# Performance work log

Hardware: AMD Instinct MI355X
Metric: run time of the kernel (lower is better)

Reference implementation:

```python
import jax, jax.numpy as jnp
import numpy as np

B, C_IN, C_OUT, H, W = 32, 64, 64, 128, 128
K, KH, KW = 4, 3, 3
HID = max(8, C_IN // 4)  # reduction=4 -> 16


def setup_inputs() -> dict:
    key = jax.random.key(0)
    ks = jax.random.split(key, 16)
    s = lambda k, shape, scale=0.1: jax.random.normal(k, shape, dtype=jnp.float32) * scale
    inp = {
        "x": jax.random.normal(ks[0], (B, C_IN, H, W), dtype=jnp.float32),
        "weight": s(ks[1], (K, C_OUT, C_IN, KH, KW)),  # static weight bank
        "bias": s(ks[2], (C_OUT,)),
        "mlp_w": s(ks[3], (HID, C_IN)),
        "mlp_b": s(ks[4], (HID,)),
        "wK": s(ks[5], (K, HID)),  "bK": s(ks[6], (K,)),
        "wO": s(ks[7], (C_OUT, HID)), "bO": s(ks[8], (C_OUT,)),
        "wI": s(ks[9], (C_IN, HID)),  "bI": s(ks[10], (C_IN,)),
        "wH": s(ks[11], (KH, HID)),   "bH": s(ks[12], (KH,)),
        "wW": s(ks[13], (KW, HID)),   "bW": s(ks[14], (KW,)),
    }
    return inp


def reference(x, weight, bias, mlp_w, mlp_b, wK, bK, wO, bO, wI, bI, wH, bH, wW, bW):
    # ---- attention branch: global avg pool -> MLP -> 5 heads ----
    g = jnp.mean(x, axis=(2, 3))                         # [B, C_in]
    h = jax.nn.relu(g @ mlp_w.T + mlp_b)                 # [B, HID]
    aK = jax.nn.softmax(h @ wK.T + bK, axis=1)           # [B, K]
    aO = jax.nn.sigmoid(h @ wO.T + bO)                   # [B, O]
    aI = jax.nn.sigmoid(h @ wI.T + bI)                   # [B, I]
    aH = jax.nn.sigmoid(h @ wH.T + bH)                   # [B, kh]
    aW = jax.nn.sigmoid(h @ wW.T + bW)                   # [B, kw]
    aH = aH / (jnp.sum(aH, axis=1, keepdims=True) + 1e-6)
    aW = aW / (jnp.sum(aW, axis=1, keepdims=True) + 1e-6)
    # fused 5-way outer product + reduction over K (same math as alpha einsum)
    w_dyn = jnp.einsum('bk,bo,bi,bh,bw,koihw->boihw', aK, aO, aI, aH, aW, weight)
    # ---- per-sample conv2d (groups=B trick expressed as vmap) ----
    def conv_one(xb, wb):
        return jax.lax.conv_general_dilated(
            xb[None], wb, window_strides=(1, 1), padding=((1, 1), (1, 1)),
            dimension_numbers=('NCHW', 'OIHW', 'NCHW'))[0]
    out = jax.vmap(conv_one)(x, w_dyn) + bias[None, :, None, None]
    return out
```

## Files before the change

### kernel.cpp

```cpp
#include <hip/hip_runtime.h>
#include <hip/hip_bf16.h>
#include <math.h>

#define BB 32
#define CI 64
#define CO 64
#define HH 128
#define WW 128
#define KK 4
#define HID 16

typedef __attribute__((ext_vector_type(8)))  __bf16 bf16x8;
typedef __attribute__((ext_vector_type(16))) float  floatx16;

__device__ __forceinline__ unsigned short f2bf(float f) {
    union { float f; unsigned int u; } a; a.f = f;
    unsigned int u = a.u;
    unsigned int r = (u + 0x7fffu + ((u >> 16) & 1u)) >> 16;
    return (unsigned short)r;
}

__global__ __launch_bounds__(256) void pool_kernel(const float* __restrict__ x,
                                                   float* __restrict__ g) {
    int bc = blockIdx.x;
    const float4* p = reinterpret_cast<const float4*>(x + (size_t)bc * (HH * WW));
    float s = 0.f;
    for (int i = threadIdx.x; i < (HH * WW) / 4; i += 256) {
        float4 v = p[i];
        s += v.x + v.y + v.z + v.w;
    }
    for (int off = 32; off > 0; off >>= 1) s += __shfl_down(s, off, 64);
    __shared__ float red[4];
    if ((threadIdx.x & 63) == 0) red[threadIdx.x >> 6] = s;
    __syncthreads();
    if (threadIdx.x == 0) {
        float tot = red[0] + red[1] + red[2] + red[3];
        g[bc] = tot * (1.0f / (HH * WW));
    }
}

__global__ __launch_bounds__(64) void attn_kernel(
    const float* __restrict__ g,
    const float* __restrict__ mlp_w, const float* __restrict__ mlp_b,
    const float* __restrict__ wK, const float* __restrict__ bK,
    const float* __restrict__ wO, const float* __restrict__ bO,
    const float* __restrict__ wI, const float* __restrict__ bI,
    const float* __restrict__ wH, const float* __restrict__ bH,
    const float* __restrict__ wW, const float* __restrict__ bW,
    float* __restrict__ aK, float* __restrict__ aO, float* __restrict__ aI,
    float* __restrict__ aH, float* __restrict__ aW) {
    int b = blockIdx.x;
    int t = threadIdx.x;
    __shared__ float sg[CI];
    __shared__ float sh[HID];
    __shared__ float sK[KK];
    __shared__ float sH[3];
    __shared__ float sW[3];

    sg[t] = g[b * CI + t];
    __syncthreads();

    if (t < HID) {
        float s = mlp_b[t];
        for (int c = 0; c < CI; c++) s = fmaf(mlp_w[t * CI + c], sg[c], s);
        sh[t] = fmaxf(s, 0.f);
    }
    __syncthreads();

    {
        float sO = bO[t], sI = bI[t];
        for (int j = 0; j < HID; j++) {
            float hv = sh[j];
            sO = fmaf(wO[t * HID + j], hv, sO);
            sI = fmaf(wI[t * HID + j], hv, sI);
        }
        aO[b * CO + t] = 1.f / (1.f + expf(-sO));
        aI[b * CI + t] = 1.f / (1.f + expf(-sI));
    }
    if (t < KK) {
        float s = bK[t];
        for (int j = 0; j < HID; j++) s = fmaf(wK[t * HID + j], sh[j], s);
        sK[t] = s;
    }
    if (t < 3) {
        float s = bH[t];
        for (int j = 0; j < HID; j++) s = fmaf(wH[t * HID + j], sh[j], s);
        sH[t] = 1.f / (1.f + expf(-s));
        float s2 = bW[t];
        for (int j = 0; j < HID; j++) s2 = fmaf(wW[t * HID + j], sh[j], s2);
        sW[t] = 1.f / (1.f + expf(-s2));
    }
    __syncthreads();

    if (t == 0) {
        float m = fmaxf(fmaxf(sK[0], sK[1]), fmaxf(sK[2], sK[3]));
        float e0 = expf(sK[0] - m), e1 = expf(sK[1] - m);
        float e2 = expf(sK[2] - m), e3 = expf(sK[3] - m);
        float s = e0 + e1 + e2 + e3;
        aK[b * KK + 0] = e0 / s;
        aK[b * KK + 1] = e1 / s;
        aK[b * KK + 2] = e2 / s;
        aK[b * KK + 3] = e3 / s;
        float hs = sH[0] + sH[1] + sH[2] + 1e-6f;
        float wsum = sW[0] + sW[1] + sW[2] + 1e-6f;
        for (int i = 0; i < 3; i++) {
            aH[b * 3 + i] = sH[i] / hs;
            aW[b * 3 + i] = sW[i] / wsum;
        }
    }
}

#define WD_TOT (BB * 9 * CO * CI)
__global__ __launch_bounds__(256) void wdyn_kernel(
    const float* __restrict__ weight,
    const float* __restrict__ aK, const float* __restrict__ aO,
    const float* __restrict__ aI, const float* __restrict__ aH,
    const float* __restrict__ aW, unsigned short* __restrict__ wdbf) {
    int idx = blockIdx.x * 256 + threadIdx.x;
    if (idx >= WD_TOT) return;
    int i   = idx & 63;
    int o   = (idx >> 6) & 63;
    int bt  = idx >> 12;
    int tap = bt % 9;
    int b   = bt / 9;

    int wbase = (o * CI + i) * 9 + tap;
    const float* ak = aK + b * KK;
    float s = 0.f;
#pragma unroll
    for (int k = 0; k < KK; k++) s = fmaf(ak[k], weight[k * (CO * CI * 9) + wbase], s);
    float v = s * aO[b * CO + o] * aI[b * CI + i] *
              aH[b * 3 + tap / 3] * aW[b * 3 + tap % 3];
    wdbf[idx] = f2bf(v);
}

#define ICCH 16
#define PADI 24
#define SX_ELE (6 * 130 * PADI)
#define SW_ELE (9 * 64 * PADI)

__global__ __launch_bounds__(512, 4) void conv_kernel(
    const float* __restrict__ x, const unsigned short* __restrict__ wdbf,
    const float* __restrict__ bias, float* __restrict__ out) {
    const int y0 = blockIdx.x * 4;
    const int b  = blockIdx.y;
    const int t  = threadIdx.x;
    const int lane = t & 63;
    const int w    = t >> 6;
    const int ry   = w >> 1;
    const int c0   = (w & 1) * 64;
    const int l31  = lane & 31;
    const int koct = lane >> 5;

    __shared__ __align__(16) unsigned short sx[SX_ELE];
    __shared__ __align__(16) unsigned short sw[SW_ELE];

    floatx16 acc[2][2];
#pragma unroll
    for (int i = 0; i < 2; i++)
#pragma unroll
        for (int j = 0; j < 2; j++)
#pragma unroll
            for (int q = 0; q < 16; q++) acc[i][j][q] = 0.f;

    const float* xb = x + (size_t)b * CI * HH * WW;
    const unsigned short* wdb = wdbf + (size_t)b * 9 * CO * CI;

    const int pA0 = (0 * 32 + l31) * PADI + koct * 8;
    const int pA1 = (1 * 32 + l31) * PADI + koct * 8;
    const int pB0 = (ry * 130 + c0 + 0  + l31) * PADI + koct * 8;
    const int pB1 = (ry * 130 + c0 + 32 + l31) * PADI + koct * 8;

    for (int chunk = 0; chunk < 4; chunk++) {
        const int ic0 = chunk * ICCH;
        __syncthreads();
        for (int idx = t; idx < 6 * 130 * 8; idx += 512) {
            int c  = idx % 130;
            int t2 = idx / 130;
            int r  = t2 % 6;
            int icp = t2 / 6;
            int gy = y0 - 1 + r;
            int gx = c - 1;
            float f0 = 0.f, f1 = 0.f;
            if ((unsigned)gy < (unsigned)HH && (unsigned)gx < (unsigned)WW) {
                const float* xp = xb + (size_t)(ic0 + icp * 2) * (HH * WW) + gy * WW + gx;
                f0 = xp[0];
                f1 = xp[HH * WW];
            }
            unsigned int pk = (unsigned int)f2bf(f0) | ((unsigned int)f2bf(f1) << 16);
            *reinterpret_cast<unsigned int*>(&sx[(r * 130 + c) * PADI + icp * 2]) = pk;
        }
        for (int idx = t; idx < 9 * 64 * 2; idx += 512) {
            int k8  = idx & 1;
            int oc  = (idx >> 1) & 63;
            int tap = idx >> 7;
            const uint4 v = *reinterpret_cast<const uint4*>(
                wdb + ((tap * 64 + oc) * 64 + ic0 + k8 * 8));
            *reinterpret_cast<uint4*>(&sw[(tap * 64 + oc) * PADI + k8 * 8]) = v;
        }
        __syncthreads();

#pragma unroll
        for (int kh = 0; kh < 3; kh++) {
#pragma unroll
            for (int kw = 0; kw < 3; kw++) {
                const int tap  = kh * 3 + kw;
                const int aoff = tap * (64 * PADI);
                const int boff = (kh * 130 + kw) * PADI;
                bf16x8 a0 = *reinterpret_cast<const bf16x8*>(&sw[pA0 + aoff]);
                bf16x8 a1 = *reinterpret_cast<const bf16x8*>(&sw[pA1 + aoff]);
                bf16x8 b0 = *reinterpret_cast<const bf16x8*>(&sx[pB0 + boff]);
                bf16x8 b1 = *reinterpret_cast<const bf16x8*>(&sx[pB1 + boff]);
                acc[0][0] = __builtin_amdgcn_mfma_f32_32x32x16_bf16(a0, b0, acc[0][0], 0, 0, 0);
                acc[0][1] = __builtin_amdgcn_mfma_f32_32x32x16_bf16(a0, b1, acc[0][1], 0, 0, 0);
                acc[1][0] = __builtin_amdgcn_mfma_f32_32x32x16_bf16(a1, b0, acc[1][0], 0, 0, 0);
                acc[1][1] = __builtin_amdgcn_mfma_f32_32x32x16_bf16(a1, b1, acc[1][1], 0, 0, 0);
            }
        }
    }

    const int y = y0 + ry;
    float* ob = out + (size_t)b * CO * HH * WW + (size_t)y * WW;
#pragma unroll
    for (int mt = 0; mt < 2; mt++) {
#pragma unroll
        for (int r = 0; r < 16; r++) {
            int oc = mt * 32 + (r & 3) + 8 * (r >> 2) + 4 * koct;
            float bv = bias[oc];
            ob[(size_t)oc * (HH * WW) + c0 + l31]      = acc[mt][0][r] + bv;
            ob[(size_t)oc * (HH * WW) + c0 + l31 + 32] = acc[mt][1][r] + bv;
        }
    }
}

extern "C" void kernel_launch(void* const* d_in, const int* in_sizes, int n_in,
                              void* d_out, int out_size, void* d_ws, size_t ws_size,
                              hipStream_t stream) {
    const float* x     = (const float*)d_in[0];
    const float* weight= (const float*)d_in[1];
    const float* bias  = (const float*)d_in[2];
    const float* mlp_w = (const float*)d_in[3];
    const float* mlp_b = (const float*)d_in[4];
    const float* wK    = (const float*)d_in[5];
    const float* bK    = (const float*)d_in[6];
    const float* wO    = (const float*)d_in[7];
    const float* bO    = (const float*)d_in[8];
    const float* wI    = (const float*)d_in[9];
    const float* bI    = (const float*)d_in[10];
    const float* wH    = (const float*)d_in[11];
    const float* bH    = (const float*)d_in[12];
    const float* wW    = (const float*)d_in[13];
    const float* bW    = (const float*)d_in[14];
    float* out = (float*)d_out;

    float* ws = (float*)d_ws;
    float* g  = ws;
    float* aK = g + 2048;
    float* aO = aK + 128;
    float* aI = aO + 2048;
    float* aH = aI + 2048;
    float* aW = aH + 96;
    unsigned short* wdbf = (unsigned short*)(ws + 8192);

    pool_kernel<<<BB * CI, 256, 0, stream>>>(x, g);
    attn_kernel<<<BB, 64, 0, stream>>>(g, mlp_w, mlp_b, wK, bK, wO, bO, wI, bI,
                                       wH, bH, wW, bW, aK, aO, aI, aH, aW);
    wdyn_kernel<<<(WD_TOT + 255) / 256, 256, 0, stream>>>(weight, aK, aO, aI, aH, aW, wdbf);
    conv_kernel<<<dim3(HH / 4, BB), 512, 0, stream>>>(x, wdbf, bias, out);
}
```

Baseline: 329.8 us.

## Fuse pooling with bf16 NHWC transpose and prefetch conv tiles into registers

Replaces the pooling kernel with one that reads x once per row, emits per-row channel sums and writes a bf16 channel-last copy of x. The conv kernel then loads 16-byte vectors from that copy instead of doing strided fp32 gathers with per-element conversion. It also prefetches the next channel chunk into registers while computing the current one. The cost is an extra bf16 write and re-read of the whole input through global memory, plus a larger workspace and more registers.

```diff
diff --git a/kernel.cpp b/kernel.cpp
--- a/kernel.cpp
+++ b/kernel.cpp
@@ -20,27 +20,54 @@
     return (unsigned short)r;
 }
 
-__global__ __launch_bounds__(256) void pool_kernel(const float* __restrict__ x,
-                                                   float* __restrict__ g) {
-    int bc = blockIdx.x;
-    const float4* p = reinterpret_cast<const float4*>(x + (size_t)bc * (HH * WW));
-    float s = 0.f;
-    for (int i = threadIdx.x; i < (HH * WW) / 4; i += 256) {
-        float4 v = p[i];
-        s += v.x + v.y + v.z + v.w;
-    }
-    for (int off = 32; off > 0; off >>= 1) s += __shfl_down(s, off, 64);
-    __shared__ float red[4];
-    if ((threadIdx.x & 63) == 0) red[threadIdx.x >> 6] = s;
-    __syncthreads();
-    if (threadIdx.x == 0) {
-        float tot = red[0] + red[1] + red[2] + red[3];
-        g[bc] = tot * (1.0f / (HH * WW));
-    }
-}
-
-__global__ __launch_bounds__(64) void attn_kernel(
-    const float* __restrict__ g,
+__global__ __launch_bounds__(256) void pooltr_kernel(const float* __restrict__ x,
+                                                     float* __restrict__ rowsum,
+                                                     unsigned short* __restrict__ xT) {
+    const int y = blockIdx.x;
+    const int b = blockIdx.y;
+    const int t = threadIdx.x;
+    __shared__ __align__(16) unsigned int sT[128 * 36];
+
+    const int ic2 = t >> 3;
+    const int q   = t & 7;
+
+    const float* xb = x + ((size_t)(b * CI + 2 * ic2) * HH + y) * WW;
+    const float4* r0 = reinterpret_cast<const float4*>(xb);
+    const float4* r1 = reinterpret_cast<const float4*>(xb + HH * WW);
+    float s0 = 0.f, s1 = 0.f;
+#pragma unroll
+    for (int it = 0; it < 4; it++) {
+        int c4 = q + it * 8;
+        float4 f0 = r0[c4];
+        float4 f1 = r1[c4];
+        s0 += f0.x + f0.y + f0.z + f0.w;
+        s1 += f1.x + f1.y + f1.z + f1.w;
+        int cb = c4 * 4;
+        sT[(cb + 0) * 36 + ic2] = (unsigned)f2bf(f0.x) | ((unsigned)f2bf(f1.x) << 16);
+        sT[(cb + 1) * 36 + ic2] = (unsigned)f2bf(f0.y) | ((unsigned)f2bf(f1.y) << 16);
+        sT[(cb + 2) * 36 + ic2] = (unsigned)f2bf(f0.z) | ((unsigned)f2bf(f1.z) << 16);
+        sT[(cb + 3) * 36 + ic2] = (unsigned)f2bf(f0.w) | ((unsigned)f2bf(f1.w) << 16);
+    }
+    s0 += __shfl_xor(s0, 1, 64); s1 += __shfl_xor(s1, 1, 64);
+    s0 += __shfl_xor(s0, 2, 64); s1 += __shfl_xor(s1, 2, 64);
+    s0 += __shfl_xor(s0, 4, 64); s1 += __shfl_xor(s1, 4, 64);
+    if (q == 0) {
+        *reinterpret_cast<float2*>(rowsum + ((size_t)b * HH + y) * CI + 2 * ic2) =
+            make_float2(s0, s1);
+    }
+    __syncthreads();
+    uint4* dst = reinterpret_cast<uint4*>(xT + ((size_t)b * HH + y) * (WW * CI));
+#pragma unroll
+    for (int jt = 0; jt < 4; jt++) {
+        int idx = t + 256 * jt;
+        int c   = idx >> 3;
+        int icq = idx & 7;
+        dst[idx] = *reinterpret_cast<uint4*>(&sT[c * 36 + icq * 4]);
+    }
+}
+
+__global__ __launch_bounds__(256) void attn_kernel(
+    const float* __restrict__ rowsum,
     const float* __restrict__ mlp_w, const float* __restrict__ mlp_b,
     const float* __restrict__ wK, const float* __restrict__ bK,
     const float* __restrict__ wO, const float* __restrict__ bO,
@@ -51,13 +78,22 @@
     float* __restrict__ aH, float* __restrict__ aW) {
     int b = blockIdx.x;
     int t = threadIdx.x;
+    __shared__ float red[4][CI];
     __shared__ float sg[CI];
     __shared__ float sh[HID];
     __shared__ float sK[KK];
     __shared__ float sH[3];
     __shared__ float sW[3];
 
-    sg[t] = g[b * CI + t];
+    {
+        int ic = t & 63, seg = t >> 6;
+        const float* rs = rowsum + (size_t)b * (HH * CI) + seg * 32 * CI + ic;
+        float s = 0.f;
+        for (int yy = 0; yy < 32; yy++) s += rs[yy * CI];
+        red[seg][ic] = s;
+    }
+    __syncthreads();
+    if (t < CI) sg[t] = (red[0][t] + red[1][t] + red[2][t] + red[3][t]) * (1.0f / (HH * WW));
     __syncthreads();
 
     if (t < HID) {
@@ -67,7 +103,7 @@
     }
     __syncthreads();
 
-    {
+    if (t < CO) {
         float sO = bO[t], sI = bI[t];
         for (int j = 0; j < HID; j++) {
             float hv = sh[j];
@@ -77,18 +113,20 @@
         aO[b * CO + t] = 1.f / (1.f + expf(-sO));
         aI[b * CI + t] = 1.f / (1.f + expf(-sI));
     }
-    if (t < KK) {
-        float s = bK[t];
-        for (int j = 0; j < HID; j++) s = fmaf(wK[t * HID + j], sh[j], s);
-        sK[t] = s;
-    }
-    if (t < 3) {
-        float s = bH[t];
-        for (int j = 0; j < HID; j++) s = fmaf(wH[t * HID + j], sh[j], s);
-        sH[t] = 1.f / (1.f + expf(-s));
-        float s2 = bW[t];
-        for (int j = 0; j < HID; j++) s2 = fmaf(wW[t * HID + j], sh[j], s2);
-        sW[t] = 1.f / (1.f + expf(-s2));
+    if (t >= 64 && t < 64 + KK) {
+        int u = t - 64;
+        float s = bK[u];
+        for (int j = 0; j < HID; j++) s = fmaf(wK[u * HID + j], sh[j], s);
+        sK[u] = s;
+    }
+    if (t >= 128 && t < 131) {
+        int u = t - 128;
+        float s = bH[u];
+        for (int j = 0; j < HID; j++) s = fmaf(wH[u * HID + j], sh[j], s);
+        sH[u] = 1.f / (1.f + expf(-s));
+        float s2 = bW[u];
+        for (int j = 0; j < HID; j++) s2 = fmaf(wW[u * HID + j], sh[j], s2);
+        sW[u] = 1.f / (1.f + expf(-s2));
     }
     __syncthreads();
 
@@ -138,9 +176,11 @@
 #define PADI 24
 #define SX_ELE (6 * 130 * PADI)
 #define SW_ELE (9 * 64 * PADI)
+#define NXLD (6 * 130 * 2)
+#define NWLD (9 * 64 * 2)
 
 __global__ __launch_bounds__(512, 4) void conv_kernel(
-    const float* __restrict__ x, const unsigned short* __restrict__ wdbf,
+    const unsigned short* __restrict__ xT, const unsigned short* __restrict__ wdbf,
     const float* __restrict__ bias, float* __restrict__ out) {
     const int y0 = blockIdx.x * 4;
     const int b  = blockIdx.y;
@@ -163,42 +203,73 @@
 #pragma unroll
             for (int q = 0; q < 16; q++) acc[i][j][q] = 0.f;
 
-    const float* xb = x + (size_t)b * CI * HH * WW;
-    const unsigned short* wdb = wdbf + (size_t)b * 9 * CO * CI;
+    const unsigned short* xb  = xT + (size_t)b * (HH * WW * CI);
+    const unsigned short* wdb = wdbf + (size_t)b * (9 * CO * CI);
+
+    int xoff[4];
+    int sxoff[4];
+#pragma unroll
+    for (int j = 0; j < 4; j++) {
+        int idx = t + 512 * j;
+        xoff[j] = -1; sxoff[j] = 0;
+        if (idx < NXLD) {
+            int half = idx & 1, pix = idx >> 1;
+            int r = pix / 130, c = pix - r * 130;
+            int gy = y0 - 1 + r, gx = c - 1;
+            sxoff[j] = pix * PADI + half * 8;
+            if ((unsigned)gy < (unsigned)HH && (unsigned)gx < (unsigned)WW)
+                xoff[j] = (gy * WW + gx) * CI + half * 8;
+        }
+    }
+    int woff[3], swoff[3];
+#pragma unroll
+    for (int j = 0; j < 3; j++) {
+        int idx = t + 512 * j;
+        woff[j] = 0; swoff[j] = 0;
+        if (idx < NWLD) {
+            int k8 = idx & 1, oi = idx >> 1;
+            woff[j]  = oi * 64 + k8 * 8;
+            swoff[j] = oi * PADI + k8 * 8;
+        }
+    }
+
+    uint4 vx[4], vw[3];
+    auto issue = [&](int chunk) {
+        const int co = chunk * ICCH;
+#pragma unroll
+        for (int j = 0; j < 4; j++) {
+            vx[j] = make_uint4(0u, 0u, 0u, 0u);
+            if (xoff[j] >= 0)
+                vx[j] = *reinterpret_cast<const uint4*>(xb + xoff[j] + co);
+        }
+#pragma unroll
+        for (int j = 0; j < 3; j++) {
+            if (t + 512 * j < NWLD)
+                vw[j] = *reinterpret_cast<const uint4*>(wdb + woff[j] + co);
+        }
+    };
+    auto commit = [&]() {
+#pragma unroll
+        for (int j = 0; j < 4; j++)
+            if (t + 512 * j < NXLD)
+                *reinterpret_cast<uint4*>(&sx[sxoff[j]]) = vx[j];
+#pragma unroll
+        for (int j = 0; j < 3; j++)
+            if (t + 512 * j < NWLD)
+                *reinterpret_cast<uint4*>(&sw[swoff[j]]) = vw[j];
+    };
 
     const int pA0 = (0 * 32 + l31) * PADI + koct * 8;
     const int pA1 = (1 * 32 + l31) * PADI + koct * 8;
     const int pB0 = (ry * 130 + c0 + 0  + l31) * PADI + koct * 8;
     const int pB1 = (ry * 130 + c0 + 32 + l31) * PADI + koct * 8;
 
+    issue(0);
     for (int chunk = 0; chunk < 4; chunk++) {
-        const int ic0 = chunk * ICCH;
         __syncthreads();
-        for (int idx = t; idx < 6 * 130 * 8; idx += 512) {
-            int c  = idx % 130;
-            int t2 = idx / 130;
-            int r  = t2 % 6;
-            int icp = t2 / 6;
-            int gy = y0 - 1 + r;
-            int gx = c - 1;
-            float f0 = 0.f, f1 = 0.f;
-            if ((unsigned)gy < (unsigned)HH && (unsigned)gx < (unsigned)WW) {
-                const float* xp = xb + (size_t)(ic0 + icp * 2) * (HH * WW) + gy * WW + gx;
-                f0 = xp[0];
-                f1 = xp[HH * WW];
-            }
-            unsigned int pk = (unsigned int)f2bf(f0) | ((unsigned int)f2bf(f1) << 16);
-            *reinterpret_cast<unsigned int*>(&sx[(r * 130 + c) * PADI + icp * 2]) = pk;
-        }
-        for (int idx = t; idx < 9 * 64 * 2; idx += 512) {
-            int k8  = idx & 1;
-            int oc  = (idx >> 1) & 63;
-            int tap = idx >> 7;
-            const uint4 v = *reinterpret_cast<const uint4*>(
-                wdb + ((tap * 64 + oc) * 64 + ic0 + k8 * 8));
-            *reinterpret_cast<uint4*>(&sw[(tap * 64 + oc) * PADI + k8 * 8]) = v;
-        }
+        commit();
         __syncthreads();
+        if (chunk < 3) issue(chunk + 1);
 
 #pragma unroll
         for (int kh = 0; kh < 3; kh++) {
@@ -254,17 +325,18 @@
     float* out = (float*)d_out;
 
     float* ws = (float*)d_ws;
-    float* g  = ws;
-    float* aK = g + 2048;
+    float* rowsum = ws;
+    float* aK = ws + 262144;
     float* aO = aK + 128;
     float* aI = aO + 2048;
     float* aH = aI + 2048;
     float* aW = aH + 96;
-    unsigned short* wdbf = (unsigned short*)(ws + 8192);
-
-    pool_kernel<<<BB * CI, 256, 0, stream>>>(x, g);
-    attn_kernel<<<BB, 64, 0, stream>>>(g, mlp_w, mlp_b, wK, bK, wO, bO, wI, bI,
-                                       wH, bH, wW, bW, aK, aO, aI, aH, aW);
+    unsigned short* wdbf = (unsigned short*)(ws + 266560);
+    unsigned short* xT   = (unsigned short*)(ws + 856384);
+
+    pooltr_kernel<<<dim3(HH, BB), 256, 0, stream>>>(x, rowsum, xT);
+    attn_kernel<<<BB, 256, 0, stream>>>(rowsum, mlp_w, mlp_b, wK, bK, wO, bO,
+                                        wI, bI, wH, bH, wW, bW, aK, aO, aI, aH, aW);
     wdyn_kernel<<<(WD_TOT + 255) / 256, 256, 0, stream>>>(weight, aK, aO, aI, aH, aW, wdbf);
-    conv_kernel<<<dim3(HH / 4, BB), 512, 0, stream>>>(x, wdbf, bias, out);
-}
+    conv_kernel<<<dim3(HH / 4, BB), 512, 0, stream>>>(xT, wdbf, bias, out);
+}
```

Result: slower. 367.9 us (+11.6%).
